# Kernel optimization log

Measured on AMD Instinct MI355X. Metric: run time of the kernel, lower is better.

The kernel has to match this reference:

```python
import jax, jax.numpy as jnp
import numpy as np

N, K, DN, DA, H = 20000, 16, 128, 128, 256
D_IN = DN + DA  # 256


def _lin_init(key, out_dim, in_dim):
    scale = 1.0 / np.sqrt(in_dim)
    return jax.random.uniform(key, (out_dim, in_dim), jnp.float32, -scale, scale)


def setup_inputs() -> dict:
    key = jax.random.key(0)
    ks = jax.random.split(key, 16)
    # adjacency: col 0 = parent index; cols 1..K = neighbor indices, -1 padded.
    parent = jax.random.randint(ks[0], (N, 1), 0, N, dtype=jnp.int32)
    nbr_first = jax.random.randint(ks[1], (N, 1), 0, N, dtype=jnp.int32)  # guarantee >=1 nbr
    nbr_rest = jax.random.randint(ks[2], (N, K - 1), -1, N, dtype=jnp.int32)
    adj = jnp.concatenate([parent, nbr_first, nbr_rest], axis=1)
    names = jax.random.normal(ks[3], (N, DN), jnp.float32)
    attrs = jax.random.normal(ks[4], (N, DA), jnp.float32)
    return {
        "nodeAdjacencySpecTensor": adj,
        "nodeNamesEncoded": names,
        "nodeAttributesEncoded": attrs,
        "W_in": _lin_init(ks[5], H, D_IN),
        "b_in": jnp.zeros((H,), jnp.float32),
        "W_parent": _lin_init(ks[6], H, H),
        "b_parent": jnp.zeros((H,), jnp.float32),
        "W_neighbor": _lin_init(ks[7], H, H),
        "b_neighbor": jnp.zeros((H,), jnp.float32),
        "W_ih": _lin_init(ks[8], 3 * H, H),
        "b_ih": jnp.zeros((3 * H,), jnp.float32),
        "W_hh": _lin_init(ks[9], 3 * H, H),
        "b_hh": jnp.zeros((3 * H,), jnp.float32),
        "depth": 3,
    }


def _gru_cell(x, h, W_ih, b_ih, W_hh, b_hh):
    # torch.nn.GRUCell math; gate order r, z, n.
    gi = x @ W_ih.T + b_ih
    gh = h @ W_hh.T + b_hh
    i_r, i_z, i_n = jnp.split(gi, 3, axis=-1)
    h_r, h_z, h_n = jnp.split(gh, 3, axis=-1)
    r = jax.nn.sigmoid(i_r + h_r)
    z = jax.nn.sigmoid(i_z + h_z)
    n = jnp.tanh(i_n + r * h_n)
    return (1.0 - z) * n + z * h


def reference(nodeAdjacencySpecTensor, nodeNamesEncoded, nodeAttributesEncoded,
              W_in, b_in, W_parent, b_parent, W_neighbor, b_neighbor,
              W_ih, b_ih, W_hh, b_hh, depth):
    adj = nodeAdjacencySpecTensor
    parent_idx = adj[:, 0]                 # [N]
    nbr_idx = adj[:, 1:]                   # [N, K], -1 padded
    mask = (nbr_idx >= 0)                  # [N, K]
    safe_nbr = jnp.clip(nbr_idx, 0, None)
    nbr_count = jnp.maximum(mask.sum(axis=1), 1).astype(jnp.float32)  # [N]

    node_info = jnp.concatenate([nodeNamesEncoded, nodeAttributesEncoded], axis=-1)
    x = node_info @ W_in.T + b_in          # [N, H]

    for _ in range(depth):
        p = x @ W_parent.T + b_parent      # [N, H]
        nbr = x @ W_neighbor.T + b_neighbor  # [N, H]
        # irregular gathers
        parent_feat = p[parent_idx]        # [N, H]
        gathered = nbr[safe_nbr]           # [N, K, H]
        nbr_sum = jnp.sum(gathered * mask[:, :, None], axis=1)  # [N, H]
        summary = parent_feat + nbr_sum / nbr_count[:, None]
        x = _gru_cell(x, summary, W_ih, b_ih, W_hh, b_hh)
    return x
```

## Files before the change

### kernel.cpp

```cpp
#include <hip/hip_runtime.h>
#include <hip/hip_bf16.h>

typedef __bf16 bf16x8 __attribute__((ext_vector_type(8)));
typedef __bf16 bf16x4 __attribute__((ext_vector_type(4)));
typedef float  f32x4  __attribute__((ext_vector_type(4)));

#define NN   20000
#define NADJ 17

__device__ __forceinline__ void xcd_remap(int b, int nwg, int col_shift, int& r, int& c)
{
    int q = nwg >> 3, rem = nwg & 7;
    int x = b & 7, k = b >> 3;
    int start = x * q + (x < rem ? x : rem);
    int idx = start + k;
    r = idx >> col_shift;
    c = idx & ((1 << col_shift) - 1);
}

__global__ void pack_weights_kernel(const float* __restrict__ Win, const float* __restrict__ bin,
                                    const float* __restrict__ Wp,  const float* __restrict__ bp,
                                    const float* __restrict__ Wn,  const float* __restrict__ bn,
                                    const float* __restrict__ Wih, const float* __restrict__ bih,
                                    const float* __restrict__ Whh, const float* __restrict__ bhh,
                                    __bf16* __restrict__ Wb, float* __restrict__ bc)
{
    int idx = blockIdx.x * 256 + threadIdx.x;
    if (idx < 1536) {
        int c = idx; float v;
        if (c < 256)      v = bin[c];
        else if (c < 512) { int j = c - 256; v = bp[j] + bn[j]; }
        else {
            int rel = c - 512;
            int j = (rel >> 6) * 16 + (rel & 15);
            int g = (rel >> 4) & 3;
            if      (g == 0) v = bih[j] + bhh[j];
            else if (g == 1) v = bih[256 + j] + bhh[256 + j];
            else if (g == 2) v = bih[512 + j];
            else             v = bhh[512 + j];
        }
        bc[c] = v;
    }
    if (idx >= 180224) return;
    int e = idx << 2;
    const float* src = nullptr;
    bool zero = false;
    if (e < 65536) {
        int row = e >> 8, k = e & 255;
        src = Win + (size_t)row * 256 + k;
    } else if (e < 196608) {
        int rel = e - 65536;
        int row = rel >> 9, k = rel & 511;
        src = (k < 256) ? (Wp + (size_t)row * 256 + k)
                        : (Wn + (size_t)row * 256 + (k - 256));
    } else {
        int rel = e - 196608;
        int row = rel >> 9, k = rel & 511;
        int j = (row >> 6) * 16 + (row & 15);
        int g = (row >> 4) & 3;
        if (k < 256) {
            if (g == 3) zero = true;
            else {
                int off = (g == 0) ? 0 : (g == 1) ? 256 : 512;
                src = Wih + (size_t)(off + j) * 256 + k;
            }
        } else {
            int k2 = k - 256;
            if (g == 2) zero = true;
            else {
                int off = (g == 0) ? 0 : (g == 1) ? 256 : 512;
                src = Whh + (size_t)(off + j) * 256 + k2;
            }
        }
    }
    float4 v = zero ? make_float4(0.f, 0.f, 0.f, 0.f) : *(const float4*)src;
    bf16x4 o = { (__bf16)v.x, (__bf16)v.y, (__bf16)v.z, (__bf16)v.w };
    *(bf16x4*)(Wb + (size_t)e) = o;
}

__global__ void pack_info_kernel(const float* __restrict__ names, const float* __restrict__ attrs,
                                 __bf16* __restrict__ xb)
{
    int idx = blockIdx.x * 256 + threadIdx.x;
    if (idx >= NN * 64) return;
    int i  = idx >> 6;
    int d4 = (idx & 63) << 2;
    const float* src = (d4 < 128) ? (names + (size_t)i * 128 + d4)
                                  : (attrs + (size_t)i * 128 + (d4 - 128));
    float4 v = *(const float4*)src;
    bf16x4 o = { (__bf16)v.x, (__bf16)v.y, (__bf16)v.z, (__bf16)v.w };
    *(bf16x4*)(xb + (size_t)i * 256 + d4) = o;
}

__global__ void gather_avg_kernel(const int* __restrict__ adj, const __bf16* __restrict__ x,
                                  __bf16* __restrict__ G2)
{
    const int node = blockIdx.x * 4 + (threadIdx.x >> 6);
    const int l = threadIdx.x & 63;
    int av = (l < NADJ) ? adj[(size_t)node * NADJ + l] : -1;
    float s0 = 0.f, s1 = 0.f, s2 = 0.f, s3 = 0.f;
    int cnt = 0;
#pragma unroll
    for (int j = 1; j < NADJ; ++j) {
        int idx = __shfl(av, j, 64);
        if (idx >= 0) {
            ++cnt;
            bf16x4 v = *(const bf16x4*)(x + (size_t)idx * 256 + l * 4);
            s0 += (float)v[0]; s1 += (float)v[1]; s2 += (float)v[2]; s3 += (float)v[3];
        }
    }
    float inv = 1.f / (float)(cnt < 1 ? 1 : cnt);
    bf16x4 o = { (__bf16)(s0 * inv), (__bf16)(s1 * inv), (__bf16)(s2 * inv), (__bf16)(s3 * inv) };
    *(bf16x4*)(G2 + (size_t)node * 256 + l * 4) = o;
}

__global__ __launch_bounds__(256, 6)
void gemm_bias_kernel(const __bf16* __restrict__ A0, const __bf16* __restrict__ A1, int lda,
                      const int* __restrict__ parents, int par_stride,
                      const __bf16* __restrict__ W, int ldw,
                      const float* __restrict__ bias,
                      __bf16* __restrict__ Cb, __bf16* __restrict__ Cl,
                      int n_rows, int n_cols, int kt_n, int nwg, int col_shift)
{
    __shared__ __align__(16) __bf16 As[64 * 64];
    __shared__ __align__(16) __bf16 Bs[128 * 64];
    __shared__ int par_s[64];
    const int t = threadIdx.x;
    const int w = t >> 6;
    const int l = t & 63;
    int rb, cb_;
    xcd_remap(blockIdx.x, nwg, col_shift, rb, cb_);
    const int brow = rb * 64;
    const int bcol = cb_ * 128;
    const int wr = (w >> 1) * 32, wc = (w & 1) * 64;

    if (parents) {
        if (t < 64) {
            int node = brow + t; if (node > n_rows - 1) node = n_rows - 1;
            par_s[t] = parents[(size_t)node * par_stride];
        }
        __syncthreads();
    }

    f32x4 acc[2][4] = {};

    for (int kt = 0; kt < kt_n; ++kt) {
        const int k0 = kt * 64;
#pragma unroll
        for (int i = 0; i < 2; ++i) {
            int f   = i * 256 + t;
            int row = f >> 3;
            int cs  = ((f & 7) * 16) ^ ((row & 7) << 4);
            int ar  = brow + row; if (ar > n_rows - 1) ar = n_rows - 1;
            const __bf16* abase;
            if (parents && k0 < 256)             abase = A0 + (size_t)par_s[row] * 256 + k0;
            else if (A1 != nullptr && k0 >= 256) abase = A1 + (size_t)ar * 256 + (k0 - 256);
            else                                 abase = A0 + (size_t)ar * lda + k0;
            const __bf16* ga = abase + (cs >> 1);
            char* la = (char*)As + (i * 256 + w * 64) * 16;
            __builtin_amdgcn_global_load_lds(
                (const __attribute__((address_space(1))) unsigned int*)ga,
                (__attribute__((address_space(3))) unsigned int*)la, 16, 0, 0);
        }
#pragma unroll
        for (int i = 0; i < 4; ++i) {
            int f   = i * 256 + t;
            int row = f >> 3;
            int cs  = ((f & 7) * 16) ^ ((row & 7) << 4);
            const __bf16* gb = W + (size_t)(bcol + row) * ldw + k0 + (cs >> 1);
            char* lb = (char*)Bs + (i * 256 + w * 64) * 16;
            __builtin_amdgcn_global_load_lds(
                (const __attribute__((address_space(1))) unsigned int*)gb,
                (__attribute__((address_space(3))) unsigned int*)lb, 16, 0, 0);
        }
        asm volatile("s_waitcnt vmcnt(0)" ::: "memory");
        __syncthreads();
#pragma unroll
        for (int ks = 0; ks < 2; ++ks) {
            bf16x8 af[2], bfv[4];
#pragma unroll
            for (int m = 0; m < 2; ++m) {
                int row = wr + m * 16 + (l & 15);
                int cb  = (ks * 64 + ((l >> 4) * 16)) ^ ((row & 7) << 4);
                af[m] = *(const bf16x8*)((const char*)As + row * 128 + cb);
            }
#pragma unroll
            for (int n = 0; n < 4; ++n) {
                int row = wc + n * 16 + (l & 15);
                int cb  = (ks * 64 + ((l >> 4) * 16)) ^ ((row & 7) << 4);
                bfv[n] = *(const bf16x8*)((const char*)Bs + row * 128 + cb);
            }
#pragma unroll
            for (int m = 0; m < 2; ++m)
#pragma unroll
                for (int n = 0; n < 4; ++n)
                    acc[m][n] = __builtin_amdgcn_mfma_f32_16x16x32_bf16(af[m], bfv[n], acc[m][n], 0, 0, 0);
        }
        __syncthreads();
    }
#pragma unroll
    for (int m = 0; m < 2; ++m) {
        int r0 = brow + wr + m * 16 + ((l >> 4) * 4);
#pragma unroll
        for (int n = 0; n < 4; ++n) {
            int c = bcol + wc + n * 16 + (l & 15);
            float bv = bias[c];
#pragma unroll
            for (int i = 0; i < 4; ++i) {
                int r = r0 + i;
                if (r < n_rows) {
                    float v = acc[m][n][i] + bv;
                    __bf16 hi = (__bf16)v;
                    Cb[(size_t)r * n_cols + c] = hi;
                    if (Cl) Cl[(size_t)r * n_cols + c] = (__bf16)(v - (float)hi);
                }
            }
        }
    }
}

__global__ __launch_bounds__(256, 6)
void gru_gemm_kernel(const __bf16* __restrict__ A0, const __bf16* __restrict__ A1,
                     const __bf16* __restrict__ W,
                     const float* __restrict__ bias,
                     const __bf16* __restrict__ sbh, const __bf16* __restrict__ sbl,
                     float* __restrict__ X, __bf16* __restrict__ xb_next,
                     int n_rows)
{
    __shared__ __align__(16) __bf16 As[64 * 64];
    __shared__ __align__(16) __bf16 Bs[128 * 64];
    const int t = threadIdx.x;
    const int w = t >> 6;
    const int l = t & 63;
    int rb, cb_;
    xcd_remap(blockIdx.x, 313 * 8, 3, rb, cb_);
    const int brow = rb * 64;
    const int bcol = cb_ * 128;
    const int wr = (w >> 1) * 32, wc = (w & 1) * 64;

    f32x4 acc[2][4] = {};

    for (int kt = 0; kt < 8; ++kt) {
        const int k0 = kt * 64;
        const int skipn = (kt < 4) ? 3 : 2;
        const __bf16* ab = (kt < 4) ? (A0 + k0) : (A1 + (k0 - 256));
#pragma unroll
        for (int i = 0; i < 2; ++i) {
            int f   = i * 256 + t;
            int row = f >> 3;
            int cs  = ((f & 7) * 16) ^ ((row & 7) << 4);
            int ar  = brow + row; if (ar > n_rows - 1) ar = n_rows - 1;
            const __bf16* ga = ab + (size_t)ar * 256 + (cs >> 1);
            char* la = (char*)As + (i * 256 + w * 64) * 16;
            __builtin_amdgcn_global_load_lds(
                (const __attribute__((address_space(1))) unsigned int*)ga,
                (__attribute__((address_space(3))) unsigned int*)la, 16, 0, 0);
        }
#pragma unroll
        for (int i = 0; i < 4; ++i) {
            int f   = i * 256 + t;
            int row = f >> 3;
            int cs  = ((f & 7) * 16) ^ ((row & 7) << 4);
            const __bf16* gb = W + (size_t)(bcol + row) * 512 + k0 + (cs >> 1);
            char* lb = (char*)Bs + (i * 256 + w * 64) * 16;
            if (((row >> 4) & 3) != skipn)
                __builtin_amdgcn_global_load_lds(
                    (const __attribute__((address_space(1))) unsigned int*)gb,
                    (__attribute__((address_space(3))) unsigned int*)lb, 16, 0, 0);
        }
        asm volatile("s_waitcnt vmcnt(0)" ::: "memory");
        __syncthreads();
#pragma unroll
        for (int ks = 0; ks < 2; ++ks) {
            bf16x8 af[2], bfv[4];
#pragma unroll
            for (int m = 0; m < 2; ++m) {
                int row = wr + m * 16 + (l & 15);
                int cb  = (ks * 64 + ((l >> 4) * 16)) ^ ((row & 7) << 4);
                af[m] = *(const bf16x8*)((const char*)As + row * 128 + cb);
            }
#pragma unroll
            for (int n = 0; n < 4; ++n) {
                if (n == skipn) continue;
                int row = wc + n * 16 + (l & 15);
                int cb  = (ks * 64 + ((l >> 4) * 16)) ^ ((row & 7) << 4);
                bfv[n] = *(const bf16x8*)((const char*)Bs + row * 128 + cb);
            }
#pragma unroll
            for (int m = 0; m < 2; ++m)
#pragma unroll
                for (int n = 0; n < 4; ++n)
                    if (n != skipn)
                        acc[m][n] = __builtin_amdgcn_mfma_f32_16x16x32_bf16(af[m], bfv[n], acc[m][n], 0, 0, 0);
        }
        __syncthreads();
    }

    const int jb = ((bcol + wc) >> 6) * 16 + (l & 15);
    const int c0 = bcol + wc + (l & 15);
    const float b0 = bias[c0], b1 = bias[c0 + 16], b2 = bias[c0 + 32], b3 = bias[c0 + 48];
#pragma unroll
    for (int m = 0; m < 2; ++m) {
        int r0 = brow + wr + m * 16 + ((l >> 4) * 4);
#pragma unroll
        for (int i = 0; i < 4; ++i) {
            int r = r0 + i;
            if (r < n_rows) {
                float gr  = acc[m][0][i] + b0;
                float gz  = acc[m][1][i] + b1;
                float gin = acc[m][2][i] + b2;
                float ghn = acc[m][3][i] + b3;
                float rg = 1.f / (1.f + __expf(-gr));
                float zg = 1.f / (1.f + __expf(-gz));
                float a2 = gin + rg * ghn;
                float tt = __expf(-2.f * fabsf(a2));
                float ng = (1.f - tt) / (1.f + tt);
                ng = (a2 < 0.f) ? -ng : ng;
                float h = (float)sbh[(size_t)r * 256 + jb] + (float)sbl[(size_t)r * 256 + jb];
                float out = (1.f - zg) * ng + zg * h;
                if (X)       X[(size_t)r * 256 + jb] = out;
                if (xb_next) xb_next[(size_t)r * 256 + jb] = (__bf16)out;
            }
        }
    }
}

extern "C" void kernel_launch(void* const* d_in, const int* in_sizes, int n_in,
                              void* d_out, int out_size, void* d_ws, size_t ws_size,
                              hipStream_t stream)
{
    const int*   adj   = (const int*)  d_in[0];
    const float* names = (const float*)d_in[1];
    const float* attrs = (const float*)d_in[2];
    const float* Win = (const float*)d_in[3];
    const float* bin = (const float*)d_in[4];
    const float* Wp  = (const float*)d_in[5];
    const float* bp  = (const float*)d_in[6];
    const float* Wn  = (const float*)d_in[7];
    const float* bn  = (const float*)d_in[8];
    const float* Wih = (const float*)d_in[9];
    const float* bih = (const float*)d_in[10];
    const float* Whh = (const float*)d_in[11];
    const float* bhh = (const float*)d_in[12];
    float* X = (float*)d_out;

    char* w = (char*)d_ws;
    __bf16* xinfo = (__bf16*)(w);
    __bf16* xb0   = (__bf16*)(w + 10240000);
    __bf16* xb1   = (__bf16*)(w + 20480000);
    __bf16* sbh   = (__bf16*)(w + 30720000);
    __bf16* sbl   = (__bf16*)(w + 40960000);
    __bf16* G2    = (__bf16*)(w + 51200000);
    __bf16* Wb    = (__bf16*)(w + 61440000);
    float*  bc    = (float*) (w + 62881792);

    pack_weights_kernel<<<704, 256, 0, stream>>>(Win, bin, Wp, bp, Wn, bn, Wih, bih, Whh, bhh, Wb, bc);
    pack_info_kernel<<<5000, 256, 0, stream>>>(names, attrs, xinfo);

    gemm_bias_kernel<<<626, 256, 0, stream>>>(xinfo, nullptr, 256, nullptr, 0,
                                              Wb, 256, bc, xb0, nullptr, NN, 256, 4, 626, 1);

    __bf16* cur = xb0;
    __bf16* nxt = xb1;
    for (int d = 0; d < 3; ++d) {
        gather_avg_kernel<<<5000, 256, 0, stream>>>(adj, cur, G2);
        gemm_bias_kernel<<<626, 256, 0, stream>>>(cur, G2, 256, adj, NADJ,
                                                  Wb + 65536, 512, bc + 256,
                                                  sbh, sbl, NN, 256, 8, 626, 1);
        gru_gemm_kernel<<<2504, 256, 0, stream>>>(cur, sbh, Wb + 196608, bc + 512,
                                                  sbh, sbl, (d == 2) ? X : nullptr,
                                                  (d < 2) ? nxt : nullptr, NN);
        __bf16* tmp = cur; cur = nxt; nxt = tmp;
    }
}
```

Measured before the change: 253.0 us.

## Double-buffer LDS tiles in GEMM kernels to overlap loads with MFMA

Both GEMM kernels now keep two LDS buffers and issue the global-to-LDS loads for the next K tile before computing on the current one. A partial vmcnt wait replaces the full drain, so load latency can overlap with MFMA work. This doubles LDS use per block and lowers the launch-bounds occupancy hint from 6 to 3. In the GRU kernel the skip of unused weight sub-tiles was removed, so it now loads those weights even though they are never used.

```diff
diff --git a/kernel.cpp b/kernel.cpp
--- a/kernel.cpp
+++ b/kernel.cpp
@@ -114,7 +114,14 @@
     *(bf16x4*)(G2 + (size_t)node * 256 + l * 4) = o;
 }
 
-__global__ __launch_bounds__(256, 6)
+#define PIPE_BARRIER()                                \
+    do {                                              \
+        asm volatile("" ::: "memory");                \
+        __builtin_amdgcn_s_barrier();                 \
+        asm volatile("" ::: "memory");                \
+    } while (0)
+
+__global__ __launch_bounds__(256, 3)
 void gemm_bias_kernel(const __bf16* __restrict__ A0, const __bf16* __restrict__ A1, int lda,
                       const int* __restrict__ parents, int par_stride,
                       const __bf16* __restrict__ W, int ldw,
@@ -122,8 +129,8 @@
                       __bf16* __restrict__ Cb, __bf16* __restrict__ Cl,
                       int n_rows, int n_cols, int kt_n, int nwg, int col_shift)
 {
-    __shared__ __align__(16) __bf16 As[64 * 64];
-    __shared__ __align__(16) __bf16 Bs[128 * 64];
+    __shared__ __align__(16) __bf16 As[2][64 * 64];
+    __shared__ __align__(16) __bf16 Bs[2][128 * 64];
     __shared__ int par_s[64];
     const int t = threadIdx.x;
     const int w = t >> 6;
@@ -142,9 +149,7 @@
         __syncthreads();
     }
 
-    f32x4 acc[2][4] = {};
-
-    for (int kt = 0; kt < kt_n; ++kt) {
+    auto stage = [&](int kt, int buf) {
         const int k0 = kt * 64;
 #pragma unroll
         for (int i = 0; i < 2; ++i) {
@@ -157,7 +162,7 @@
             else if (A1 != nullptr && k0 >= 256) abase = A1 + (size_t)ar * 256 + (k0 - 256);
             else                                 abase = A0 + (size_t)ar * lda + k0;
             const __bf16* ga = abase + (cs >> 1);
-            char* la = (char*)As + (i * 256 + w * 64) * 16;
+            char* la = (char*)As[buf] + (i * 256 + w * 64) * 16;
             __builtin_amdgcn_global_load_lds(
                 (const __attribute__((address_space(1))) unsigned int*)ga,
                 (__attribute__((address_space(3))) unsigned int*)la, 16, 0, 0);
@@ -168,13 +173,25 @@
             int row = f >> 3;
             int cs  = ((f & 7) * 16) ^ ((row & 7) << 4);
             const __bf16* gb = W + (size_t)(bcol + row) * ldw + k0 + (cs >> 1);
-            char* lb = (char*)Bs + (i * 256 + w * 64) * 16;
+            char* lb = (char*)Bs[buf] + (i * 256 + w * 64) * 16;
             __builtin_amdgcn_global_load_lds(
                 (const __attribute__((address_space(1))) unsigned int*)gb,
                 (__attribute__((address_space(3))) unsigned int*)lb, 16, 0, 0);
         }
-        asm volatile("s_waitcnt vmcnt(0)" ::: "memory");
-        __syncthreads();
+    };
+
+    f32x4 acc[2][4] = {};
+    stage(0, 0);
+
+    for (int kt = 0; kt < kt_n; ++kt) {
+        const int buf = kt & 1;
+        if (kt + 1 < kt_n) {
+            stage(kt + 1, buf ^ 1);
+            asm volatile("s_waitcnt vmcnt(6)" ::: "memory");
+        } else {
+            asm volatile("s_waitcnt vmcnt(0)" ::: "memory");
+        }
+        PIPE_BARRIER();
 #pragma unroll
         for (int ks = 0; ks < 2; ++ks) {
             bf16x8 af[2], bfv[4];
@@ -182,13 +199,13 @@
             for (int m = 0; m < 2; ++m) {
                 int row = wr + m * 16 + (l & 15);
                 int cb  = (ks * 64 + ((l >> 4) * 16)) ^ ((row & 7) << 4);
-                af[m] = *(const bf16x8*)((const char*)As + row * 128 + cb);
+                af[m] = *(const bf16x8*)((const char*)As[buf] + row * 128 + cb);
             }
 #pragma unroll
             for (int n = 0; n < 4; ++n) {
                 int row = wc + n * 16 + (l & 15);
                 int cb  = (ks * 64 + ((l >> 4) * 16)) ^ ((row & 7) << 4);
-                bfv[n] = *(const bf16x8*)((const char*)Bs + row * 128 + cb);
+                bfv[n] = *(const bf16x8*)((const char*)Bs[buf] + row * 128 + cb);
             }
 #pragma unroll
             for (int m = 0; m < 2; ++m)
@@ -196,7 +213,7 @@
                 for (int n = 0; n < 4; ++n)
                     acc[m][n] = __builtin_amdgcn_mfma_f32_16x16x32_bf16(af[m], bfv[n], acc[m][n], 0, 0, 0);
         }
-        __syncthreads();
+        PIPE_BARRIER();
     }
 #pragma unroll
     for (int m = 0; m < 2; ++m) {
@@ -219,7 +236,7 @@
     }
 }
 
-__global__ __launch_bounds__(256, 6)
+__global__ __launch_bounds__(256, 3)
 void gru_gemm_kernel(const __bf16* __restrict__ A0, const __bf16* __restrict__ A1,
                      const __bf16* __restrict__ W,
                      const float* __restrict__ bias,
@@ -227,8 +244,8 @@
                      float* __restrict__ X, __bf16* __restrict__ xb_next,
                      int n_rows)
 {
-    __shared__ __align__(16) __bf16 As[64 * 64];
-    __shared__ __align__(16) __bf16 Bs[128 * 64];
+    __shared__ __align__(16) __bf16 As[2][64 * 64];
+    __shared__ __align__(16) __bf16 Bs[2][128 * 64];
     const int t = threadIdx.x;
     const int w = t >> 6;
     const int l = t & 63;
@@ -238,11 +255,8 @@
     const int bcol = cb_ * 128;
     const int wr = (w >> 1) * 32, wc = (w & 1) * 64;
 
-    f32x4 acc[2][4] = {};
-
-    for (int kt = 0; kt < 8; ++kt) {
+    auto stage = [&](int kt, int buf) {
         const int k0 = kt * 64;
-        const int skipn = (kt < 4) ? 3 : 2;
         const __bf16* ab = (kt < 4) ? (A0 + k0) : (A1 + (k0 - 256));
 #pragma unroll
         for (int i = 0; i < 2; ++i) {
@@ -251,7 +265,7 @@
             int cs  = ((f & 7) * 16) ^ ((row & 7) << 4);
             int ar  = brow + row; if (ar > n_rows - 1) ar = n_rows - 1;
             const __bf16* ga = ab + (size_t)ar * 256 + (cs >> 1);
-            char* la = (char*)As + (i * 256 + w * 64) * 16;
+            char* la = (char*)As[buf] + (i * 256 + w * 64) * 16;
             __builtin_amdgcn_global_load_lds(
                 (const __attribute__((address_space(1))) unsigned int*)ga,
                 (__attribute__((address_space(3))) unsigned int*)la, 16, 0, 0);
@@ -262,14 +276,26 @@
             int row = f >> 3;
             int cs  = ((f & 7) * 16) ^ ((row & 7) << 4);
             const __bf16* gb = W + (size_t)(bcol + row) * 512 + k0 + (cs >> 1);
-            char* lb = (char*)Bs + (i * 256 + w * 64) * 16;
-            if (((row >> 4) & 3) != skipn)
-                __builtin_amdgcn_global_load_lds(
-                    (const __attribute__((address_space(1))) unsigned int*)gb,
-                    (__attribute__((address_space(3))) unsigned int*)lb, 16, 0, 0);
-        }
-        asm volatile("s_waitcnt vmcnt(0)" ::: "memory");
-        __syncthreads();
+            char* lb = (char*)Bs[buf] + (i * 256 + w * 64) * 16;
+            __builtin_amdgcn_global_load_lds(
+                (const __attribute__((address_space(1))) unsigned int*)gb,
+                (__attribute__((address_space(3))) unsigned int*)lb, 16, 0, 0);
+        }
+    };
+
+    f32x4 acc[2][4] = {};
+    stage(0, 0);
+
+    for (int kt = 0; kt < 8; ++kt) {
+        const int buf = kt & 1;
+        const int skipn = (kt < 4) ? 3 : 2;
+        if (kt < 7) {
+            stage(kt + 1, buf ^ 1);
+            asm volatile("s_waitcnt vmcnt(6)" ::: "memory");
+        } else {
+            asm volatile("s_waitcnt vmcnt(0)" ::: "memory");
+        }
+        PIPE_BARRIER();
 #pragma unroll
         for (int ks = 0; ks < 2; ++ks) {
             bf16x8 af[2], bfv[4];
@@ -277,14 +303,14 @@
             for (int m = 0; m < 2; ++m) {
                 int row = wr + m * 16 + (l & 15);
                 int cb  = (ks * 64 + ((l >> 4) * 16)) ^ ((row & 7) << 4);
-                af[m] = *(const bf16x8*)((const char*)As + row * 128 + cb);
+                af[m] = *(const bf16x8*)((const char*)As[buf] + row * 128 + cb);
             }
 #pragma unroll
             for (int n = 0; n < 4; ++n) {
                 if (n == skipn) continue;
                 int row = wc + n * 16 + (l & 15);
                 int cb  = (ks * 64 + ((l >> 4) * 16)) ^ ((row & 7) << 4);
-                bfv[n] = *(const bf16x8*)((const char*)Bs + row * 128 + cb);
+                bfv[n] = *(const bf16x8*)((const char*)Bs[buf] + row * 128 + cb);
             }
 #pragma unroll
             for (int m = 0; m < 2; ++m)
@@ -293,7 +319,7 @@
                     if (n != skipn)
                         acc[m][n] = __builtin_amdgcn_mfma_f32_16x16x32_bf16(af[m], bfv[n], acc[m][n], 0, 0, 0);
         }
-        __syncthreads();
+        PIPE_BARRIER();
     }
 
     const int jb = ((bcol + wc) >> 6) * 16 + (l & 15);
```

After: 248.6 us. About the same (-1.7%).
